# Kernel tuning notes

Hardware: AMD Instinct MI355X
Metric: run time of the kernel (lower is better)

The kernel has to match this reference:

```python
import jax, jax.numpy as jnp
import numpy as np

HEAD_DIM = 128
PROJ_DIM = 64


def setup_inputs() -> dict:
    key = jax.random.key(0)
    kq, kk, kv, kr = jax.random.split(key, 4)
    B, H, NQ, NKV = 1, 16, 2048, 4096
    Q = jax.random.normal(kq, (B, H, NQ, HEAD_DIM), dtype=jnp.float32)
    K = jax.random.normal(kk, (B, H, NKV, HEAD_DIM), dtype=jnp.float32)
    V = jax.random.normal(kv, (B, H, NKV, HEAD_DIM), dtype=jnp.float32)
    # R ~ N(0,1) / sqrt(proj_dim), as in the torch __init__
    R = jax.random.normal(kr, (HEAD_DIM, PROJ_DIM), dtype=jnp.float32) / (PROJ_DIM ** 0.5)
    return {"Q": Q, "K": K, "V": V, "R": R}


def reference(Q, K, V, R):
    proj_dim = R.shape[-1]
    scale = 1.0 / (proj_dim ** 0.5)
    # Project Q and K into the random-projection space: [B,H,N,proj_dim]
    Q_proj = jnp.einsum('bhnd,dp->bhnp', Q, R)
    K_proj = jnp.einsum('bhmd,dp->bhmp', K, R)
    # scores: [B,H,NQ,NKV]
    scores = jnp.einsum('bhnp,bhmp->bhnm', Q_proj, K_proj) * scale
    weights = jax.nn.softmax(scores, axis=-1)
    # output: [B,H,NQ,head_dim]
    return jnp.einsum('bhnm,bhmd->bhnd', weights, V)
```

## Files before the change

### kernel.cpp

```cpp
#include <hip/hip_runtime.h>

#define HEADS 16
#define NQ    2048
#define NKV   4096
#define DH    128
#define PDIM  64

typedef __bf16 bf16_t;
typedef bf16_t bf16x8 __attribute__((ext_vector_type(8)));
typedef bf16_t bf16x4 __attribute__((ext_vector_type(4)));
typedef bf16_t bf16x2 __attribute__((ext_vector_type(2)));
typedef float  f32x4  __attribute__((ext_vector_type(4)));
typedef float  f32x16 __attribute__((ext_vector_type(16)));
typedef int    i32x4  __attribute__((ext_vector_type(4)));

typedef __attribute__((address_space(3))) unsigned int       lds_u32;
typedef __attribute__((address_space(1))) const unsigned int glb_u32;

__device__ __forceinline__ void dma16(const void* g, void* l) {
  __builtin_amdgcn_global_load_lds((glb_u32*)g, (lds_u32*)l, 16, 0, 0);
}

__global__ __launch_bounds__(256) void prep_kernel(
    const float* __restrict__ Q, const float* __restrict__ K,
    const float* __restrict__ V, const float* __restrict__ R,
    bf16_t* __restrict__ Qp, bf16_t* __restrict__ Kp, bf16_t* __restrict__ Vt)
{
  __shared__ float  sF[64 * 132];
  __shared__ bf16_t sY[4][16 * 72];
  const int tid = threadIdx.x;
  const int bid = blockIdx.x;

  const int isQ = (bid < 512);
  const int isK = (bid >= 512) && (bid < 1536);

  const float* src;
  long row0;
  if (isQ)      { src = Q; row0 = (long)bid * 64; }
  else if (isK) { src = K; row0 = (long)(bid - 512) * 64; }
  else          { src = V; row0 = (long)(bid - 1536) * 64; }
  const float* tp = src + row0 * DH;
#pragma unroll
  for (int rep = 0; rep < 8; ++rep) {
    const int slot = tid + rep * 256;
    const int j = slot >> 5, c4 = (slot & 31) * 4;
    f32x4 v = *(const f32x4*)(tp + j * DH + c4);
    *(f32x4*)(&sF[j * 132 + c4]) = v;
  }
  __syncthreads();

  if (!isQ && !isK) {
    const int vb = bid - 1536;
    const int h = vb >> 6, jt = vb & 63;
    bf16_t* op = Vt + (long)h * DH * NKV + jt * 64;
#pragma unroll
    for (int rep = 0; rep < 4; ++rep) {
      const int slot = tid + rep * 256;
      const int d = slot >> 3, j8 = (slot & 7) * 8;
      bf16x8 w;
#pragma unroll
      for (int jj = 0; jj < 8; ++jj) w[jj] = (bf16_t)sF[(j8 + jj) * 132 + d];
      *(bf16x8*)(op + (long)d * NKV + j8) = w;
    }
    return;
  }

  const int wave = tid >> 6, lane = tid & 63;
  const int n16  = lane & 15, quad = lane >> 4;
  const float scale = isQ ? 0.18033688011112042f : 1.0f;
  bf16_t* Y = isQ ? Qp : Kp;

  bf16x8 bfr[4][4];
#pragma unroll
  for (int nt = 0; nt < 4; ++nt) {
    const int n = nt * 16 + n16;
#pragma unroll
    for (int kk = 0; kk < 4; ++kk) {
      const int k0 = kk * 32 + quad * 8;
      bf16x8 b;
#pragma unroll
      for (int j = 0; j < 8; ++j) b[j] = (bf16_t)R[(k0 + j) * PDIM + n];
      bfr[nt][kk] = b;
    }
  }

  const int arow = wave * 16 + n16;
  bf16x8 a[4];
#pragma unroll
  for (int kk = 0; kk < 4; ++kk) {
    const int k0 = kk * 32 + quad * 8;
    f32x4 x0 = *(const f32x4*)(&sF[arow * 132 + k0]);
    f32x4 x1 = *(const f32x4*)(&sF[arow * 132 + k0 + 4]);
    bf16x8 av;
#pragma unroll
    for (int j = 0; j < 4; ++j) { av[j] = (bf16_t)(x0[j] * scale); av[4 + j] = (bf16_t)(x1[j] * scale); }
    a[kk] = av;
  }

  bf16_t* sy = sY[wave];
#pragma unroll
  for (int nt = 0; nt < 4; ++nt) {
    f32x4 acc = {0.f, 0.f, 0.f, 0.f};
#pragma unroll
    for (int kk = 0; kk < 4; ++kk)
      acc = __builtin_amdgcn_mfma_f32_16x16x32_bf16(a[kk], bfr[nt][kk], acc, 0, 0, 0);
#pragma unroll
    for (int r = 0; r < 4; ++r)
      sy[(quad * 4 + r) * 72 + nt * 16 + n16] = (bf16_t)acc[r];
  }
  const long xrow = row0 + wave * 16;
  const int row = lane >> 2, cg = lane & 3;
  bf16x8 w0 = *(const bf16x8*)(&sy[row * 72 + cg * 16]);
  bf16x8 w1 = *(const bf16x8*)(&sy[row * 72 + cg * 16 + 8]);
  *(bf16x8*)(Y + (xrow + row) * PDIM + cg * 16)     = w0;
  *(bf16x8*)(Y + (xrow + row) * PDIM + cg * 16 + 8) = w1;
}

__global__ __launch_bounds__(128, 2) void flash_kernel(
    const bf16_t* __restrict__ Qp, const bf16_t* __restrict__ Kp,
    const bf16_t* __restrict__ Vt, bf16_t* __restrict__ Opart,
    float* __restrict__ Lpart, float* __restrict__ Out,
    int splits, int iters)
{
  __shared__ char smem[24576];
  bf16_t* sK = (bf16_t*)smem;
  bf16_t* sV = (bf16_t*)(smem + 8192);

  const int tid  = threadIdx.x;
  const int wave = tid >> 6, lane = tid & 63;
  const int l31  = lane & 31, h = lane >> 5;

  const int head = blockIdx.x & 15;
  const int qt   = (blockIdx.x >> 4) & 15;
  const int sp   = blockIdx.x >> 8;

  const int qbase = qt * 128 + wave * 64;
  const int kv0   = sp * (64 * iters);

  bf16x8 qf[2][4];
#pragma unroll
  for (int qsub = 0; qsub < 2; ++qsub)
#pragma unroll
    for (int k = 0; k < 4; ++k)
      qf[qsub][k] = *(const bf16x8*)(Qp + ((long)head * NQ + qbase + qsub * 32 + l31) * PDIM
                                     + k * 16 + h * 8);

  f32x16 o[2][4] = {};
  float rsum[2] = {0.f, 0.f};

  const bf16_t* kpH = Kp + (long)head * NKV * PDIM;
  const bf16_t* vtH = Vt + (long)head * DH * NKV;

  const int sw = ((lane & 7) ^ ((lane >> 3) & 7)) * 8;
  const int r8 = lane >> 3;

  for (int t = 0; t < iters; ++t) {
    const int kvb = kv0 + t * 64;
    __syncthreads();
    if (wave == 0) {
#pragma unroll
      for (int i = 0; i < 8; ++i)
        dma16(kpH + (long)(kvb + i * 8 + r8) * PDIM + sw, smem + i * 1024);
#pragma unroll
      for (int i = 0; i < 4; ++i)
        dma16(vtH + (long)(i * 8 + r8) * NKV + kvb + sw, smem + 8192 + i * 1024);
    } else {
#pragma unroll
      for (int i = 4; i < 16; ++i)
        dma16(vtH + (long)(i * 8 + r8) * NKV + kvb + sw, smem + 8192 + i * 1024);
    }
    __syncthreads();

#pragma unroll
    for (int s = 0; s < 2; ++s) {
      int bfr[2][2][4];
#pragma unroll
      for (int qsub = 0; qsub < 2; ++qsub) {
        f32x16 sc = {};
        const int r = s * 32 + l31;
#pragma unroll
        for (int k = 0; k < 4; ++k) {
          const int c = 2 * k + h;
          const bf16x8 a = *(const bf16x8*)(sK + r * 64 + ((c ^ (r & 7)) * 8));
          sc = __builtin_amdgcn_mfma_f32_32x32x16_bf16(a, qf[qsub][k], sc, 0, 0, 0);
        }
        int pk[4][2];
#pragma unroll
        for (int rg = 0; rg < 4; ++rg) {
          const float p0 = __builtin_amdgcn_exp2f(sc[rg * 4 + 0]);
          const float p1 = __builtin_amdgcn_exp2f(sc[rg * 4 + 1]);
          const float p2 = __builtin_amdgcn_exp2f(sc[rg * 4 + 2]);
          const float p3 = __builtin_amdgcn_exp2f(sc[rg * 4 + 3]);
          rsum[qsub] += (p0 + p1) + (p2 + p3);
          union { bf16x2 v; int i; } u0, u1;
          u0.v = bf16x2{(bf16_t)p0, (bf16_t)p1};
          u1.v = bf16x2{(bf16_t)p2, (bf16_t)p3};
          pk[rg][0] = u0.i; pk[rg][1] = u1.i;
        }
#pragma unroll
        for (int cl = 0; cl < 2; ++cl) {
          const int e00 = __shfl_xor(pk[2 * cl][0], 32);
          const int e01 = __shfl_xor(pk[2 * cl][1], 32);
          const int e10 = __shfl_xor(pk[2 * cl + 1][0], 32);
          const int e11 = __shfl_xor(pk[2 * cl + 1][1], 32);
          bfr[qsub][cl][0] = h ? e10 : pk[2 * cl][0];
          bfr[qsub][cl][1] = h ? e11 : pk[2 * cl][1];
          bfr[qsub][cl][2] = h ? pk[2 * cl + 1][0] : e00;
          bfr[qsub][cl][3] = h ? pk[2 * cl + 1][1] : e01;
        }
      }
#pragma unroll
      for (int dsub = 0; dsub < 4; ++dsub) {
        const int r = dsub * 32 + l31;
#pragma unroll
        for (int cl = 0; cl < 2; ++cl) {
          const int c = 2 * (2 * s + cl) + h;
          const bf16x8 va = *(const bf16x8*)(sV + r * 64 + ((c ^ (r & 7)) * 8));
#pragma unroll
          for (int qsub = 0; qsub < 2; ++qsub) {
            union { i32x4 i; bf16x8 v; } pb;
            pb.i = i32x4{bfr[qsub][cl][0], bfr[qsub][cl][1],
                         bfr[qsub][cl][2], bfr[qsub][cl][3]};
            o[qsub][dsub] = __builtin_amdgcn_mfma_f32_32x32x16_bf16(va, pb.v, o[qsub][dsub], 0, 0, 0);
          }
        }
      }
    }
  }

  __syncthreads();
  bf16_t* myT = (bf16_t*)(smem + wave * 8704);
#pragma unroll
  for (int qsub = 0; qsub < 2; ++qsub) {
    const float lsum = rsum[qsub] + __shfl_xor(rsum[qsub], 32);
    const float scale = (splits > 1) ? 1.0f : (1.0f / lsum);
#pragma unroll
    for (int dsub = 0; dsub < 4; ++dsub)
#pragma unroll
      for (int rg = 0; rg < 4; ++rg) {
        bf16x4 w = { (bf16_t)(o[qsub][dsub][rg * 4 + 0] * scale),
                     (bf16_t)(o[qsub][dsub][rg * 4 + 1] * scale),
                     (bf16_t)(o[qsub][dsub][rg * 4 + 2] * scale),
                     (bf16_t)(o[qsub][dsub][rg * 4 + 3] * scale) };
        *(bf16x4*)(myT + l31 * 136 + dsub * 32 + rg * 8 + h * 4) = w;
      }
    const int qglob = qbase + qsub * 32;
#pragma unroll
    for (int j = 0; j < 8; ++j) {
      const int ql = j * 4 + (lane >> 4);
      bf16x8 v = *(const bf16x8*)(myT + ql * 136 + (lane & 15) * 8);
      if (splits > 1) {
        *(bf16x8*)(Opart + (((long)sp * HEADS + head) * NQ + qglob + ql) * DH + (lane & 15) * 8) = v;
      } else {
        float* op = Out + ((long)head * NQ + qglob + ql) * DH + (lane & 15) * 8;
        f32x4 a = {(float)v[0], (float)v[1], (float)v[2], (float)v[3]};
        f32x4 b = {(float)v[4], (float)v[5], (float)v[6], (float)v[7]};
        *(f32x4*)op = a; *(f32x4*)(op + 4) = b;
      }
    }
    if (splits > 1 && h == 0)
      Lpart[((long)sp * HEADS + head) * NQ + qglob + l31] = lsum;
  }
}

__global__ __launch_bounds__(256) void combine_kernel(
    const bf16_t* __restrict__ Opart, const float* __restrict__ Lpart,
    float* __restrict__ Out)
{
  const long idx = (long)blockIdx.x * 256 + threadIdx.x;
  const int  d8  = (int)(idx & 15);
  const long hq  = idx >> 4;
  float l = 0.f;
  float acc[8];
#pragma unroll
  for (int j = 0; j < 8; ++j) acc[j] = 0.f;
#pragma unroll
  for (int s = 0; s < 4; ++s) {
    l += Lpart[s * (long)(HEADS * NQ) + hq];
    bf16x8 v = *(const bf16x8*)(Opart + (s * (long)(HEADS * NQ) + hq) * DH + d8 * 8);
#pragma unroll
    for (int j = 0; j < 8; ++j) acc[j] += (float)v[j];
  }
  const float inv = 1.f / l;
  f32x4 o0 = { acc[0] * inv, acc[1] * inv, acc[2] * inv, acc[3] * inv };
  f32x4 o1 = { acc[4] * inv, acc[5] * inv, acc[6] * inv, acc[7] * inv };
  float* op = Out + hq * DH + d8 * 8;
  *(f32x4*)(op)     = o0;
  *(f32x4*)(op + 4) = o1;
}

extern "C" void kernel_launch(void* const* d_in, const int* in_sizes, int n_in,
                              void* d_out, int out_size, void* d_ws, size_t ws_size,
                              hipStream_t stream)
{
  const float* Q = (const float*)d_in[0];
  const float* K = (const float*)d_in[1];
  const float* V = (const float*)d_in[2];
  const float* R = (const float*)d_in[3];
  float* Out = (float*)d_out;

  char* ws = (char*)d_ws;
  bf16_t* Qp = (bf16_t*)(ws);
  bf16_t* Kp = (bf16_t*)(ws + (size_t)(4  << 20));
  bf16_t* Vt = (bf16_t*)(ws + (size_t)(12 << 20));
  bf16_t* Opart = (bf16_t*)(ws + (size_t)(28 << 20));
  float*  Lpart = (float*)(ws + (size_t)(60 << 20));

  const size_t need4 = (size_t)(60 << 20) + 4ull * HEADS * NQ * sizeof(float);
  const int splits = (ws_size >= need4) ? 4 : 1;
  const int iters  = NKV / (64 * splits);

  prep_kernel<<<2560, 256, 0, stream>>>(Q, K, V, R, Qp, Kp, Vt);
  flash_kernel<<<splits * 256, 128, 0, stream>>>(Qp, Kp, Vt, Opart, Lpart, Out,
                                                 splits, iters);
  if (splits == 4)
    combine_kernel<<<2048, 256, 0, stream>>>(Opart, Lpart, Out);
}
```

Before: 193.9 us.

## Double-buffer K/V tiles in LDS with 4-wave blocks and MFMA priority hints

Blocks grow from two waves to four, covering 256 query rows, so each K/V tile staged in LDS is reused by twice as many waves. The K/V staging now goes to two LDS buffers: the next tile is prefetched while the current one is computed, and a waitcnt plus barrier at the end of each iteration replaces the two syncthreads per step. s_setprio raises wave priority around the MFMA sections. LDS use doubles to 48KB per block, and the grid halves, which may lower occupancy and the number of blocks per CU.

```diff
diff --git a/kernel.cpp b/kernel.cpp
--- a/kernel.cpp
+++ b/kernel.cpp
@@ -116,25 +116,23 @@
   *(bf16x8*)(Y + (xrow + row) * PDIM + cg * 16 + 8) = w1;
 }
 
-__global__ __launch_bounds__(128, 2) void flash_kernel(
+__global__ __launch_bounds__(256, 2) void flash_kernel(
     const bf16_t* __restrict__ Qp, const bf16_t* __restrict__ Kp,
     const bf16_t* __restrict__ Vt, bf16_t* __restrict__ Opart,
     float* __restrict__ Lpart, float* __restrict__ Out,
     int splits, int iters)
 {
-  __shared__ char smem[24576];
-  bf16_t* sK = (bf16_t*)smem;
-  bf16_t* sV = (bf16_t*)(smem + 8192);
+  __shared__ char smem[49152];
 
   const int tid  = threadIdx.x;
   const int wave = tid >> 6, lane = tid & 63;
   const int l31  = lane & 31, h = lane >> 5;
 
   const int head = blockIdx.x & 15;
-  const int qt   = (blockIdx.x >> 4) & 15;
-  const int sp   = blockIdx.x >> 8;
-
-  const int qbase = qt * 128 + wave * 64;
+  const int qt   = (blockIdx.x >> 4) & 7;
+  const int sp   = blockIdx.x >> 7;
+
+  const int qbase = qt * 256 + wave * 64;
   const int kv0   = sp * (64 * iters);
 
   bf16x8 qf[2][4];
@@ -154,22 +152,30 @@
   const int sw = ((lane & 7) ^ ((lane >> 3) & 7)) * 8;
   const int r8 = lane >> 3;
 
+  auto STAGE = [&](char* dst, int kvb) {
+#pragma unroll
+    for (int i = 0; i < 6; ++i) {
+      const int d = wave * 6 + i;
+      if (d < 8)
+        dma16(kpH + (long)(kvb + d * 8 + r8) * PDIM + sw, dst + d * 1024);
+      else
+        dma16(vtH + (long)((d - 8) * 8 + r8) * NKV + kvb + sw,
+              dst + 8192 + (d - 8) * 1024);
+    }
+  };
+
+  STAGE(smem, kv0);
+  asm volatile("s_waitcnt vmcnt(0)" ::: "memory");
+  __builtin_amdgcn_s_barrier();
+  asm volatile("" ::: "memory");
+
   for (int t = 0; t < iters; ++t) {
-    const int kvb = kv0 + t * 64;
-    __syncthreads();
-    if (wave == 0) {
-#pragma unroll
-      for (int i = 0; i < 8; ++i)
-        dma16(kpH + (long)(kvb + i * 8 + r8) * PDIM + sw, smem + i * 1024);
-#pragma unroll
-      for (int i = 0; i < 4; ++i)
-        dma16(vtH + (long)(i * 8 + r8) * NKV + kvb + sw, smem + 8192 + i * 1024);
-    } else {
-#pragma unroll
-      for (int i = 4; i < 16; ++i)
-        dma16(vtH + (long)(i * 8 + r8) * NKV + kvb + sw, smem + 8192 + i * 1024);
-    }
-    __syncthreads();
+    char* cur = smem + ((t & 1) ? 24576 : 0);
+    if (t + 1 < iters)
+      STAGE(smem + ((t & 1) ? 0 : 24576), kv0 + (t + 1) * 64);
+
+    bf16_t* sK = (bf16_t*)cur;
+    bf16_t* sV = (bf16_t*)(cur + 8192);
 
 #pragma unroll
     for (int s = 0; s < 2; ++s) {
@@ -178,12 +184,14 @@
       for (int qsub = 0; qsub < 2; ++qsub) {
         f32x16 sc = {};
         const int r = s * 32 + l31;
+        __builtin_amdgcn_s_setprio(1);
 #pragma unroll
         for (int k = 0; k < 4; ++k) {
           const int c = 2 * k + h;
           const bf16x8 a = *(const bf16x8*)(sK + r * 64 + ((c ^ (r & 7)) * 8));
           sc = __builtin_amdgcn_mfma_f32_32x32x16_bf16(a, qf[qsub][k], sc, 0, 0, 0);
         }
+        __builtin_amdgcn_s_setprio(0);
         int pk[4][2];
 #pragma unroll
         for (int rg = 0; rg < 4; ++rg) {
@@ -209,6 +217,7 @@
           bfr[qsub][cl][3] = h ? pk[2 * cl + 1][1] : e01;
         }
       }
+      __builtin_amdgcn_s_setprio(1);
 #pragma unroll
       for (int dsub = 0; dsub < 4; ++dsub) {
         const int r = dsub * 32 + l31;
@@ -225,7 +234,12 @@
           }
         }
       }
-    }
+      __builtin_amdgcn_s_setprio(0);
+    }
+
+    asm volatile("s_waitcnt vmcnt(0)" ::: "memory");
+    __builtin_amdgcn_s_barrier();
+    asm volatile("" ::: "memory");
   }
 
   __syncthreads();
@@ -311,7 +325,7 @@
   const int iters  = NKV / (64 * splits);
 
   prep_kernel<<<2560, 256, 0, stream>>>(Q, K, V, R, Qp, Kp, Vt);
-  flash_kernel<<<splits * 256, 128, 0, stream>>>(Qp, Kp, Vt, Opart, Lpart, Out,
+  flash_kernel<<<splits * 128, 256, 0, stream>>>(Qp, Kp, Vt, Opart, Lpart, Out,
                                                  splits, iters);
   if (splits == 4)
     combine_kernel<<<2048, 256, 0, stream>>>(Opart, Lpart, Out);
```

Result: slower. 280.2 us (+44.5%).

## Enlarge flash tiles to 256 queries x 128 keys and swizzle prep LDS

Applied to the files above, without the earlier changes.

The flash kernel now runs 4 waves per block over 256 query rows and loads 128 keys per iteration, so each K/V tile in LDS is shared by twice as many queries and the number of barrier-separated iterations is halved. The DMA distribution and V swizzle are reworked for the wider 128-column V tile. Separately, the prep kernel's padded LDS staging buffer is replaced by an XOR-swizzled layout to avoid bank conflicts without padding. The grid halves to 512 blocks and LDS per block doubles to 48KB, which may reduce occupancy and wave-level parallelism.

```diff
diff --git a/kernel.cpp b/kernel.cpp
--- a/kernel.cpp
+++ b/kernel.cpp
@@ -26,7 +26,7 @@
     const float* __restrict__ V, const float* __restrict__ R,
     bf16_t* __restrict__ Qp, bf16_t* __restrict__ Kp, bf16_t* __restrict__ Vt)
 {
-  __shared__ float  sF[64 * 132];
+  __shared__ float  sF[64 * 128];
   __shared__ bf16_t sY[4][16 * 72];
   const int tid = threadIdx.x;
   const int bid = blockIdx.x;
@@ -43,9 +43,9 @@
 #pragma unroll
   for (int rep = 0; rep < 8; ++rep) {
     const int slot = tid + rep * 256;
-    const int j = slot >> 5, c4 = (slot & 31) * 4;
-    f32x4 v = *(const f32x4*)(tp + j * DH + c4);
-    *(f32x4*)(&sF[j * 132 + c4]) = v;
+    const int j = slot >> 5, g = slot & 31;
+    f32x4 v = *(const f32x4*)(tp + j * DH + g * 4);
+    *(f32x4*)(&sF[j * 128 + ((g ^ ((j >> 3) & 7)) << 2)]) = v;
   }
   __syncthreads();
 
@@ -57,9 +57,11 @@
     for (int rep = 0; rep < 4; ++rep) {
       const int slot = tid + rep * 256;
       const int d = slot >> 3, j8 = (slot & 7) * 8;
+      const int key = slot & 7;
+      const int gsw = (((d >> 2) ^ key) << 2) + (d & 3);
       bf16x8 w;
 #pragma unroll
-      for (int jj = 0; jj < 8; ++jj) w[jj] = (bf16_t)sF[(j8 + jj) * 132 + d];
+      for (int jj = 0; jj < 8; ++jj) w[jj] = (bf16_t)sF[(j8 + jj) * 128 + gsw];
       *(bf16x8*)(op + (long)d * NKV + j8) = w;
     }
     return;
@@ -85,12 +87,14 @@
   }
 
   const int arow = wave * 16 + n16;
+  const int akey = (arow >> 3) & 7;
   bf16x8 a[4];
 #pragma unroll
   for (int kk = 0; kk < 4; ++kk) {
     const int k0 = kk * 32 + quad * 8;
-    f32x4 x0 = *(const f32x4*)(&sF[arow * 132 + k0]);
-    f32x4 x1 = *(const f32x4*)(&sF[arow * 132 + k0 + 4]);
+    const int g0 = k0 >> 2;
+    f32x4 x0 = *(const f32x4*)(&sF[arow * 128 + ((g0 ^ akey) << 2)]);
+    f32x4 x1 = *(const f32x4*)(&sF[arow * 128 + (((g0 + 1) ^ akey) << 2)]);
     bf16x8 av;
 #pragma unroll
     for (int j = 0; j < 4; ++j) { av[j] = (bf16_t)(x0[j] * scale); av[4 + j] = (bf16_t)(x1[j] * scale); }
@@ -116,26 +120,26 @@
   *(bf16x8*)(Y + (xrow + row) * PDIM + cg * 16 + 8) = w1;
 }
 
-__global__ __launch_bounds__(128, 2) void flash_kernel(
+__global__ __launch_bounds__(256, 2) void flash_kernel(
     const bf16_t* __restrict__ Qp, const bf16_t* __restrict__ Kp,
     const bf16_t* __restrict__ Vt, bf16_t* __restrict__ Opart,
     float* __restrict__ Lpart, float* __restrict__ Out,
     int splits, int iters)
 {
-  __shared__ char smem[24576];
+  __shared__ char smem[49152];
   bf16_t* sK = (bf16_t*)smem;
-  bf16_t* sV = (bf16_t*)(smem + 8192);
+  bf16_t* sV = (bf16_t*)(smem + 16384);
 
   const int tid  = threadIdx.x;
   const int wave = tid >> 6, lane = tid & 63;
   const int l31  = lane & 31, h = lane >> 5;
 
   const int head = blockIdx.x & 15;
-  const int qt   = (blockIdx.x >> 4) & 15;
-  const int sp   = blockIdx.x >> 8;
-
-  const int qbase = qt * 128 + wave * 64;
-  const int kv0   = sp * (64 * iters);
+  const int qt   = (blockIdx.x >> 4) & 7;
+  const int sp   = blockIdx.x >> 7;
+
+  const int qbase = qt * 256 + wave * 64;
+  const int kv0   = sp * (128 * iters);
 
   bf16x8 qf[2][4];
 #pragma unroll
@@ -151,28 +155,40 @@
   const bf16_t* kpH = Kp + (long)head * NKV * PDIM;
   const bf16_t* vtH = Vt + (long)head * DH * NKV;
 
-  const int sw = ((lane & 7) ^ ((lane >> 3) & 7)) * 8;
-  const int r8 = lane >> 3;
+  const int r8  = lane >> 3;
+  const int r4  = lane >> 4;
+  const int swK  = ((lane & 7) ^ r8) * 8;
+  const int swV0 = ((lane & 15) ^ r4) * 8;
+  const int swV1 = ((lane & 15) ^ (4 + r4)) * 8;
 
   for (int t = 0; t < iters; ++t) {
-    const int kvb = kv0 + t * 64;
+    const int kvb = kv0 + t * 128;
     __syncthreads();
     if (wave == 0) {
 #pragma unroll
-      for (int i = 0; i < 8; ++i)
-        dma16(kpH + (long)(kvb + i * 8 + r8) * PDIM + sw, smem + i * 1024);
-#pragma unroll
-      for (int i = 0; i < 4; ++i)
-        dma16(vtH + (long)(i * 8 + r8) * NKV + kvb + sw, smem + 8192 + i * 1024);
+      for (int i = 0; i < 12; ++i)
+        dma16(kpH + (long)(kvb + i * 8 + r8) * PDIM + swK, smem + i * 1024);
+    } else if (wave == 1) {
+#pragma unroll
+      for (int i = 12; i < 16; ++i)
+        dma16(kpH + (long)(kvb + i * 8 + r8) * PDIM + swK, smem + i * 1024);
+#pragma unroll
+      for (int j = 0; j < 8; ++j)
+        dma16(vtH + (long)(j * 4 + r4) * NKV + kvb + ((j & 1) ? swV1 : swV0),
+              smem + 16384 + j * 1024);
     } else {
-#pragma unroll
-      for (int i = 4; i < 16; ++i)
-        dma16(vtH + (long)(i * 8 + r8) * NKV + kvb + sw, smem + 8192 + i * 1024);
+      const int j0 = (wave - 2) * 12 + 8;
+#pragma unroll
+      for (int i = 0; i < 12; ++i) {
+        const int j = j0 + i;
+        dma16(vtH + (long)(j * 4 + r4) * NKV + kvb + ((j & 1) ? swV1 : swV0),
+              smem + 16384 + j * 1024);
+      }
     }
     __syncthreads();
 
 #pragma unroll
-    for (int s = 0; s < 2; ++s) {
+    for (int s = 0; s < 4; ++s) {
       int bfr[2][2][4];
 #pragma unroll
       for (int qsub = 0; qsub < 2; ++qsub) {
@@ -215,7 +231,7 @@
 #pragma unroll
         for (int cl = 0; cl < 2; ++cl) {
           const int c = 2 * (2 * s + cl) + h;
-          const bf16x8 va = *(const bf16x8*)(sV + r * 64 + ((c ^ (r & 7)) * 8));
+          const bf16x8 va = *(const bf16x8*)(sV + r * 128 + ((c ^ (r & 7)) * 8));
 #pragma unroll
           for (int qsub = 0; qsub < 2; ++qsub) {
             union { i32x4 i; bf16x8 v; } pb;
@@ -308,10 +324,10 @@
 
   const size_t need4 = (size_t)(60 << 20) + 4ull * HEADS * NQ * sizeof(float);
   const int splits = (ws_size >= need4) ? 4 : 1;
-  const int iters  = NKV / (64 * splits);
+  const int iters  = NKV / (128 * splits);
 
   prep_kernel<<<2560, 256, 0, stream>>>(Q, K, V, R, Qp, Kp, Vt);
-  flash_kernel<<<splits * 256, 128, 0, stream>>>(Qp, Kp, Vt, Opart, Lpart, Out,
+  flash_kernel<<<splits * 128, 256, 0, stream>>>(Qp, Kp, Vt, Opart, Lpart, Out,
                                                  splits, iters);
   if (splits == 4)
     combine_kernel<<<2048, 256, 0, stream>>>(Opart, Lpart, Out);
```

Result: slower. 351.8 us (+81.4%).

## Split prep into R pre-transpose, direct-load projection, and swizzled V transpose kernels

Applied to the files above, without the earlier changes.

The fused prep kernel is split into three kernels. A one-block kernel converts R to a transposed bf16 copy once, replacing the per-block scalar reads of fp32 R. The Q/K projection now loads rows straight from global memory into registers with no LDS staging. The V transpose uses an XOR-swizzled LDS layout to avoid bank conflicts. The cost is two extra kernel launches, and the Rbt buffer shares workspace with Opart, which is safe only because it is consumed before flash writes there.

```diff
diff --git a/kernel.cpp b/kernel.cpp
--- a/kernel.cpp
+++ b/kernel.cpp
@@ -21,76 +21,51 @@
   __builtin_amdgcn_global_load_lds((glb_u32*)g, (lds_u32*)l, 16, 0, 0);
 }
 
-__global__ __launch_bounds__(256) void prep_kernel(
+__global__ __launch_bounds__(256) void rprep_kernel(
+    const float* __restrict__ R, bf16_t* __restrict__ Rbt)
+{
+  const int tid = threadIdx.x;
+#pragma unroll
+  for (int rep = 0; rep < 32; ++rep) {
+    const int idx = tid + rep * 256;
+    const int n = idx & 63, k = idx >> 6;
+    Rbt[n * 128 + k] = (bf16_t)R[k * 64 + n];
+  }
+}
+
+__global__ __launch_bounds__(256) void proj_kernel(
     const float* __restrict__ Q, const float* __restrict__ K,
-    const float* __restrict__ V, const float* __restrict__ R,
-    bf16_t* __restrict__ Qp, bf16_t* __restrict__ Kp, bf16_t* __restrict__ Vt)
-{
-  __shared__ float  sF[64 * 132];
+    const bf16_t* __restrict__ Rbt,
+    bf16_t* __restrict__ Qp, bf16_t* __restrict__ Kp)
+{
   __shared__ bf16_t sY[4][16 * 72];
   const int tid = threadIdx.x;
   const int bid = blockIdx.x;
 
   const int isQ = (bid < 512);
-  const int isK = (bid >= 512) && (bid < 1536);
-
-  const float* src;
-  long row0;
-  if (isQ)      { src = Q; row0 = (long)bid * 64; }
-  else if (isK) { src = K; row0 = (long)(bid - 512) * 64; }
-  else          { src = V; row0 = (long)(bid - 1536) * 64; }
-  const float* tp = src + row0 * DH;
-#pragma unroll
-  for (int rep = 0; rep < 8; ++rep) {
-    const int slot = tid + rep * 256;
-    const int j = slot >> 5, c4 = (slot & 31) * 4;
-    f32x4 v = *(const f32x4*)(tp + j * DH + c4);
-    *(f32x4*)(&sF[j * 132 + c4]) = v;
-  }
-  __syncthreads();
-
-  if (!isQ && !isK) {
-    const int vb = bid - 1536;
-    const int h = vb >> 6, jt = vb & 63;
-    bf16_t* op = Vt + (long)h * DH * NKV + jt * 64;
-#pragma unroll
-    for (int rep = 0; rep < 4; ++rep) {
-      const int slot = tid + rep * 256;
-      const int d = slot >> 3, j8 = (slot & 7) * 8;
-      bf16x8 w;
-#pragma unroll
-      for (int jj = 0; jj < 8; ++jj) w[jj] = (bf16_t)sF[(j8 + jj) * 132 + d];
-      *(bf16x8*)(op + (long)d * NKV + j8) = w;
-    }
-    return;
-  }
+  const float* src = isQ ? Q : K;
+  const long row0  = isQ ? (long)bid * 64 : (long)(bid - 512) * 64;
+  const float scale = isQ ? 0.18033688011112042f : 1.0f;
+  bf16_t* Y = isQ ? Qp : Kp;
 
   const int wave = tid >> 6, lane = tid & 63;
   const int n16  = lane & 15, quad = lane >> 4;
-  const float scale = isQ ? 0.18033688011112042f : 1.0f;
-  bf16_t* Y = isQ ? Qp : Kp;
 
   bf16x8 bfr[4][4];
 #pragma unroll
-  for (int nt = 0; nt < 4; ++nt) {
-    const int n = nt * 16 + n16;
-#pragma unroll
-    for (int kk = 0; kk < 4; ++kk) {
-      const int k0 = kk * 32 + quad * 8;
-      bf16x8 b;
-#pragma unroll
-      for (int j = 0; j < 8; ++j) b[j] = (bf16_t)R[(k0 + j) * PDIM + n];
-      bfr[nt][kk] = b;
-    }
-  }
+  for (int nt = 0; nt < 4; ++nt)
+#pragma unroll
+    for (int kk = 0; kk < 4; ++kk)
+      bfr[nt][kk] = *(const bf16x8*)(Rbt + (nt * 16 + n16) * 128 + kk * 32 + quad * 8);
 
   const int arow = wave * 16 + n16;
+  const float* xp = src + (row0 + arow) * DH;
   bf16x8 a[4];
 #pragma unroll
   for (int kk = 0; kk < 4; ++kk) {
     const int k0 = kk * 32 + quad * 8;
-    f32x4 x0 = *(const f32x4*)(&sF[arow * 132 + k0]);
-    f32x4 x1 = *(const f32x4*)(&sF[arow * 132 + k0 + 4]);
+    f32x4 x0 = *(const f32x4*)(xp + k0);
+    f32x4 x1 = *(const f32x4*)(xp + k0 + 4);
     bf16x8 av;
 #pragma unroll
     for (int j = 0; j < 4; ++j) { av[j] = (bf16_t)(x0[j] * scale); av[4 + j] = (bf16_t)(x1[j] * scale); }
@@ -114,6 +89,38 @@
   bf16x8 w1 = *(const bf16x8*)(&sy[row * 72 + cg * 16 + 8]);
   *(bf16x8*)(Y + (xrow + row) * PDIM + cg * 16)     = w0;
   *(bf16x8*)(Y + (xrow + row) * PDIM + cg * 16 + 8) = w1;
+}
+
+__global__ __launch_bounds__(256) void vtrans_kernel(
+    const float* __restrict__ V, bf16_t* __restrict__ Vt)
+{
+  __shared__ float sF[64 * 128];
+  const int tid = threadIdx.x;
+  const int bid = blockIdx.x;
+
+  const float* tp = V + (long)bid * 64 * DH;
+#pragma unroll
+  for (int rep = 0; rep < 8; ++rep) {
+    const int slot = tid + rep * 256;
+    const int j = slot >> 5, g = slot & 31;
+    f32x4 v = *(const f32x4*)(tp + j * DH + g * 4);
+    *(f32x4*)(&sF[j * 128 + ((g ^ ((j >> 3) & 7)) << 2)]) = v;
+  }
+  __syncthreads();
+
+  const int h = bid >> 6, jt = bid & 63;
+  bf16_t* op = Vt + (long)h * DH * NKV + jt * 64;
+#pragma unroll
+  for (int rep = 0; rep < 4; ++rep) {
+    const int slot = tid + rep * 256;
+    const int d = slot >> 3, j8 = (slot & 7) * 8;
+    const int key = slot & 7;
+    const int gsw = (((d >> 2) ^ key) << 2) + (d & 3);
+    bf16x8 w;
+#pragma unroll
+    for (int jj = 0; jj < 8; ++jj) w[jj] = (bf16_t)sF[(j8 + jj) * 128 + gsw];
+    *(bf16x8*)(op + (long)d * NKV + j8) = w;
+  }
 }
 
 __global__ __launch_bounds__(128, 2) void flash_kernel(
@@ -305,12 +312,15 @@
   bf16_t* Vt = (bf16_t*)(ws + (size_t)(12 << 20));
   bf16_t* Opart = (bf16_t*)(ws + (size_t)(28 << 20));
   float*  Lpart = (float*)(ws + (size_t)(60 << 20));
+  bf16_t* Rbt = (bf16_t*)(ws + (size_t)(28 << 20));
 
   const size_t need4 = (size_t)(60 << 20) + 4ull * HEADS * NQ * sizeof(float);
   const int splits = (ws_size >= need4) ? 4 : 1;
   const int iters  = NKV / (64 * splits);
 
-  prep_kernel<<<2560, 256, 0, stream>>>(Q, K, V, R, Qp, Kp, Vt);
+  rprep_kernel<<<1, 256, 0, stream>>>(R, Rbt);
+  proj_kernel<<<1536, 256, 0, stream>>>(Q, K, Rbt, Qp, Kp);
+  vtrans_kernel<<<1024, 256, 0, stream>>>(V, Vt);
   flash_kernel<<<splits * 256, 128, 0, stream>>>(Qp, Kp, Vt, Opart, Lpart, Out,
                                                  splits, iters);
   if (splits == 4)
```

Measured after the change: 205.2 us. 5.8% more time.
